# Performance work log

Measured on AMD Instinct MI355X. Metric: run time of the kernel, lower is better.

## Reference

```python
import jax, jax.numpy as jnp
import numpy as np

B, C, H, W = 16, 256, 128, 512
MINW, MINH, AF, HS = 128, 32, 256, 256


def _conv1d(x, w, b, pad):
    # x (B, Cin, L), w (Cout, Cin, K) -> (B, Cout, L)
    y = jax.lax.conv_general_dilated(x, w, (1,), [(pad, pad)],
                                     dimension_numbers=('NCH', 'OIH', 'NCH'))
    return y + b[None, :, None]


def setup_inputs() -> dict:
    key = jax.random.key(0)
    ks = jax.random.split(key, 22)
    def p(i, shape, s=0.05):
        return jax.random.normal(ks[i], shape, jnp.float32) * s
    return dict(
        features=jax.random.normal(ks[0], (B, C, H, W), jnp.float32),
        prev_attn_weights=jax.random.uniform(ks[1], (B, H), jnp.float32),
        coverage_vector=jax.random.uniform(ks[2], (B, H), jnp.float32) * 2.0,
        hidden=jax.random.normal(ks[3], (2, 1, B, HS), jnp.float32),
        dw_w=p(4, (MINW, 1)), dw_b=p(5, (1,)),
        enc_w=p(6, (C, AF)), enc_b=p(7, (AF,)),
        conv_w=p(8, (16, 2, 15)), conv_b=p(9, (16,)),
        dcb_w=p(10, (16, AF)), dcb_b=p(11, (AF,)),
        hid_w=p(12, (HS, AF)), hid_b=p(13, (AF,)),
        align_w=p(14, (AF, 1)), align_b=p(15, (1,)),
        convd_w=p(16, (AF, AF, 5)), convd_b=p(17, (AF,)),
        dh_w=p(18, (MINH, 1)), dh_b=p(19, (1,)),
        dec_w=p(20, (HS + AF, 2)), dec_b=p(21, (2,)),
    )


def reference(features, prev_attn_weights, coverage_vector, hidden,
              dw_w, dw_b, enc_w, enc_b, conv_w, conv_b, dcb_w, dcb_b,
              hid_w, hid_b, align_w, align_b, convd_w, convd_b,
              dh_w, dh_b, dec_w, dec_b):
    b, c, h, w = features.shape
    # AdaptiveMaxPool2d((None, MINW)): W divisible by MINW -> uniform windows
    pooled = features.reshape(b, c, h, MINW, w // MINW).max(-1)   # (B,C,H,MINW)
    h_feat = (pooled @ dw_w + dw_b)[..., 0]                       # (B,C,H)
    s = jnp.einsum('bch,cf->bhf', h_feat, enc_w) + enc_b          # (B,H,AF)
    # location + clamped coverage, InstanceNorm1d (no affine, eps=1e-5)
    cat = jnp.stack([prev_attn_weights,
                     jnp.clip(coverage_vector, 0.0, 1.0)], axis=1)  # (B,2,H)
    mu = cat.mean(-1, keepdims=True)
    var = cat.var(-1, keepdims=True)
    cat = (cat - mu) * jax.lax.rsqrt(var + 1e-5)
    cb = _conv1d(cat, conv_w, conv_b, 7)                          # (B,16,H)
    s = s + jnp.einsum('bkh,kf->bhf', cb, dcb_w) + dcb_b
    hh = hidden[0]                                                # (1,B,HS) = LSTM h
    s = s + (jnp.einsum('lbh,hf->lbf', hh, hid_w) + hid_b).transpose(1, 0, 2)  # (B,1,AF) bcast
    s = jnp.tanh(s)
    align = s @ align_w + align_b                                 # (B,H,1)
    attn = jax.nn.softmax(align, axis=1)[..., 0]                  # (B,H)
    context = jnp.einsum('bchw,bh->bcw', features, attn)          # (B,C,W)
    # learned stop decision
    d = jax.nn.relu(_conv1d(s.transpose(0, 2, 1), convd_w, convd_b, 2))  # (B,AF,H)
    d = d.reshape(b, AF, MINH, h // MINH).max(-1)                 # AdaptiveMaxPool1d(MINH)
    d = jax.nn.relu(d @ dh_w + dh_b)[..., 0]                      # (B,AF)
    d = jnp.concatenate([hh[0], d], axis=1)                       # (B,HS+AF)
    decision = d @ dec_w + dec_b                                  # (B,2)
    return context, attn, decision
```

## Files before the change

### kernel.cpp

```cpp
#include <hip/hip_runtime.h>
#include <hip/hip_bf16.h>
#include <math.h>

#define B_ 16
#define C_ 256
#define H_ 128
#define W_ 512
#define AF_ 256
#define HS_ 256

__global__ void k_pool(const float* __restrict__ feat,
                       const float* __restrict__ dw_w,
                       const float* __restrict__ dw_b,
                       float* __restrict__ hf) {
  int gid = blockIdx.x * blockDim.x + threadIdx.x;
  int wid = gid >> 6;
  int lane = threadIdx.x & 63;
  const float4* row = reinterpret_cast<const float4*>(feat) + (size_t)wid * 128;
  float4 a = row[lane];
  float4 b = row[lane + 64];
  float m0 = fmaxf(fmaxf(a.x, a.y), fmaxf(a.z, a.w));
  float m1 = fmaxf(fmaxf(b.x, b.y), fmaxf(b.z, b.w));
  float p = m0 * dw_w[lane] + m1 * dw_w[lane + 64];
#pragma unroll
  for (int off = 32; off > 0; off >>= 1) p += __shfl_down(p, off, 64);
  if (lane == 0) hf[wid] = p + dw_b[0];
}

__global__ void k_hid(const float* __restrict__ hidden,
                      const float* __restrict__ hid_w,
                      const float* __restrict__ hid_b,
                      float* __restrict__ hv) {
  int b = blockIdx.x, f = threadIdx.x;
  const float* hh = hidden + b * HS_;
  float acc = hid_b[f];
  for (int k = 0; k < HS_; ++k) acc = fmaf(hh[k], hid_w[k * AF_ + f], acc);
  hv[b * AF_ + f] = acc;
}

__global__ void k_sbuild(const float* __restrict__ pa,
                         const float* __restrict__ cv,
                         const float* __restrict__ hf,
                         const float* __restrict__ enc_w, const float* __restrict__ enc_b,
                         const float* __restrict__ conv_w, const float* __restrict__ conv_b,
                         const float* __restrict__ dcb_w, const float* __restrict__ dcb_b,
                         const float* __restrict__ hv,
                         const float* __restrict__ align_w, const float* __restrict__ align_b,
                         float* __restrict__ sbuf, float* __restrict__ alignv) {
  __shared__ float cat[2][H_];
  __shared__ float stats[4];
  __shared__ float cbl[4][16];
  __shared__ float red[4][4];
  int bidx = blockIdx.x;
  int b = bidx >> 5;
  int h0 = (bidx & 31) * 4;
  int tid = threadIdx.x;

  if (tid < H_) {
    cat[0][tid] = pa[b * H_ + tid];
    float x = cv[b * H_ + tid];
    cat[1][tid] = fminf(fmaxf(x, 0.f), 1.f);
  }
  __syncthreads();
  if (tid < 2) {
    float s = 0.f, s2 = 0.f;
    for (int t = 0; t < H_; ++t) { float x = cat[tid][t]; s += x; s2 += x * x; }
    float mu = s / (float)H_;
    float var = s2 / (float)H_ - mu * mu;
    stats[tid * 2] = mu;
    stats[tid * 2 + 1] = rsqrtf(var + 1e-5f);
  }
  __syncthreads();
  {
    int ch = tid >> 7, t = tid & 127;
    cat[ch][t] = (cat[ch][t] - stats[ch * 2]) * stats[ch * 2 + 1];
  }
  __syncthreads();
  if (tid < 64) {
    int k = tid & 15, j = tid >> 4;
    int h = h0 + j;
    float acc = conv_b[k];
    for (int c2 = 0; c2 < 2; ++c2)
      for (int t = 0; t < 15; ++t) {
        int hh = h + t - 7;
        if (hh >= 0 && hh < H_) acc += cat[c2][hh] * conv_w[(k * 2 + c2) * 15 + t];
      }
    cbl[j][k] = acc;
  }
  __syncthreads();

  int f = tid;
  float base = enc_b[f] + dcb_b[f] + hv[b * AF_ + f];
  float acc[4];
#pragma unroll
  for (int j = 0; j < 4; ++j) {
    float a = base;
#pragma unroll
    for (int k = 0; k < 16; ++k) a = fmaf(cbl[j][k], dcb_w[k * AF_ + f], a);
    acc[j] = a;
  }
  const float* hfb = hf + (size_t)(b * C_) * H_ + h0;
  for (int c = 0; c < C_; ++c) {
    float w = enc_w[c * AF_ + f];
#pragma unroll
    for (int j = 0; j < 4; ++j) acc[j] = fmaf(hfb[c * H_ + j], w, acc[j]);
  }
  float aw = align_w[f];
  int wv = tid >> 6, lane = tid & 63;
#pragma unroll
  for (int j = 0; j < 4; ++j) {
    float s = tanhf(acc[j]);
    sbuf[(size_t)(b * H_ + h0 + j) * AF_ + f] = s;
    float v = s * aw;
#pragma unroll
    for (int off = 32; off > 0; off >>= 1) v += __shfl_down(v, off, 64);
    if (lane == 0) red[wv][j] = v;
  }
  __syncthreads();
  if (tid < 4)
    alignv[b * H_ + h0 + tid] =
        red[0][tid] + red[1][tid] + red[2][tid] + red[3][tid] + align_b[0];
}

__global__ void k_softmax(const float* __restrict__ alignv, float* __restrict__ attn) {
  __shared__ float redm[2], reds[2];
  int b = blockIdx.x, t = threadIdx.x;
  float v = alignv[b * H_ + t];
  float m = v;
#pragma unroll
  for (int off = 32; off > 0; off >>= 1) m = fmaxf(m, __shfl_down(m, off, 64));
  if ((t & 63) == 0) redm[t >> 6] = m;
  __syncthreads();
  float mm = fmaxf(redm[0], redm[1]);
  float e = expf(v - mm);
  float s = e;
#pragma unroll
  for (int off = 32; off > 0; off >>= 1) s += __shfl_down(s, off, 64);
  if ((t & 63) == 0) reds[t >> 6] = s;
  __syncthreads();
  attn[b * H_ + t] = e / (reds[0] + reds[1]);
}

__global__ void k_wt(const float* __restrict__ convd_w, float* __restrict__ w2) {
  int f = blockIdx.x;
  int tid = threadIdx.x;
#pragma unroll
  for (int q = 0; q < 5; ++q) {
    int r = q * 256 + tid;
    w2[(size_t)r * 256 + f] = convd_w[(size_t)f * 1280 + r];
  }
}

__global__ void k_dconv(const float* __restrict__ sbuf, const float* __restrict__ w2,
                        const float* __restrict__ convd_b, float* __restrict__ dpool) {
  __shared__ float sw[12][AF_];
  __shared__ float part[8][AF_];
  int bidx = blockIdx.x;
  int b = bidx >> 4;
  int h0 = (bidx & 15) * 8;
  int tid = threadIdx.x;
  int f = tid & 255;
  int chalf = tid >> 8;
  for (int rr = chalf; rr < 12; rr += 2) {
    int h = h0 - 2 + rr;
    sw[rr][f] = (h >= 0 && h < H_) ? sbuf[(size_t)(b * H_ + h) * AF_ + f] : 0.f;
  }
  __syncthreads();
  float acc[8];
#pragma unroll
  for (int j = 0; j < 8; ++j) acc[j] = 0.f;
  int cstart = chalf * 128;
  for (int c = cstart; c < cstart + 128; ++c) {
    float sr[12];
#pragma unroll
    for (int rr = 0; rr < 12; ++rr) sr[rr] = sw[rr][c];
    const float* wp = w2 + (size_t)c * 5 * 256 + f;
#pragma unroll
    for (int t = 0; t < 5; ++t) {
      float wv = wp[t * 256];
#pragma unroll
      for (int j = 0; j < 8; ++j) acc[j] = fmaf(sr[j + t], wv, acc[j]);
    }
  }
  if (chalf == 1) {
#pragma unroll
    for (int j = 0; j < 8; ++j) part[j][f] = acc[j];
  }
  __syncthreads();
  if (chalf == 0) {
    float bias = convd_b[f];
#pragma unroll
    for (int j = 0; j < 8; ++j) acc[j] = fmaxf(acc[j] + part[j][f] + bias, 0.f);
    float p0 = fmaxf(fmaxf(acc[0], acc[1]), fmaxf(acc[2], acc[3]));
    float p1 = fmaxf(fmaxf(acc[4], acc[5]), fmaxf(acc[6], acc[7]));
    int m0 = h0 >> 2;
    dpool[(size_t)(b * 32 + m0) * AF_ + f] = p0;
    dpool[(size_t)(b * 32 + m0 + 1) * AF_ + f] = p1;
  }
}

__global__ void k_decision(const float* __restrict__ dpool, const float* __restrict__ hidden,
                           const float* __restrict__ dh_w, const float* __restrict__ dh_b,
                           const float* __restrict__ dec_w, const float* __restrict__ dec_b,
                           float* __restrict__ dec_out) {
  __shared__ float ddl[AF_];
  __shared__ float red[4];
  int b = blockIdx.x, tid = threadIdx.x;
  float acc = dh_b[0];
  for (int m = 0; m < 32; ++m) acc = fmaf(dpool[(size_t)(b * 32 + m) * AF_ + tid], dh_w[m], acc);
  ddl[tid] = fmaxf(acc, 0.f);
  __syncthreads();
  int col = tid >> 7, kk = tid & 127;
  float a = 0.f;
#pragma unroll
  for (int q = 0; q < 4; ++q) {
    int idx = kk + 128 * q;
    float x = (idx < 256) ? hidden[b * HS_ + idx] : ddl[idx - 256];
    a = fmaf(x, dec_w[idx * 2 + col], a);
  }
#pragma unroll
  for (int off = 32; off > 0; off >>= 1) a += __shfl_down(a, off, 64);
  if ((tid & 63) == 0) red[tid >> 6] = a;
  __syncthreads();
  if (tid < 2) dec_out[b * 2 + tid] = red[tid * 2] + red[tid * 2 + 1] + dec_b[tid];
}

__global__ void k_context(const float* __restrict__ feat, const float* __restrict__ attn,
                          float* __restrict__ ctx) {
  __shared__ float at[H_];
  int bidx = blockIdx.x;
  int b = bidx >> 7;
  int c0 = (bidx & 127) * 2;
  int tid = threadIdx.x;
  if (tid < H_) at[tid] = attn[b * H_ + tid];
  __syncthreads();
  int c = c0 + (tid >> 7);
  int wq = tid & 127;
  const float4* f4 = reinterpret_cast<const float4*>(feat) +
                     (size_t)(b * C_ + c) * H_ * (W_ / 4) + wq;
  float4 acc = make_float4(0.f, 0.f, 0.f, 0.f);
  for (int h = 0; h < H_; ++h) {
    float4 x = f4[(size_t)h * (W_ / 4)];
    float a = at[h];
    acc.x += x.x * a; acc.y += x.y * a; acc.z += x.z * a; acc.w += x.w * a;
  }
  reinterpret_cast<float4*>(ctx)[(size_t)(b * C_ + c) * (W_ / 4) + wq] = acc;
}

extern "C" void kernel_launch(void* const* d_in, const int* in_sizes, int n_in,
                              void* d_out, int out_size, void* d_ws, size_t ws_size,
                              hipStream_t stream) {
  const float* feat    = (const float*)d_in[0];
  const float* pa      = (const float*)d_in[1];
  const float* cv      = (const float*)d_in[2];
  const float* hidden  = (const float*)d_in[3];
  const float* dw_w    = (const float*)d_in[4];
  const float* dw_b    = (const float*)d_in[5];
  const float* enc_w   = (const float*)d_in[6];
  const float* enc_b   = (const float*)d_in[7];
  const float* conv_w  = (const float*)d_in[8];
  const float* conv_b  = (const float*)d_in[9];
  const float* dcb_w   = (const float*)d_in[10];
  const float* dcb_b   = (const float*)d_in[11];
  const float* hid_w   = (const float*)d_in[12];
  const float* hid_b   = (const float*)d_in[13];
  const float* align_w = (const float*)d_in[14];
  const float* align_b = (const float*)d_in[15];
  const float* convd_w = (const float*)d_in[16];
  const float* convd_b = (const float*)d_in[17];
  const float* dh_w    = (const float*)d_in[18];
  const float* dh_b    = (const float*)d_in[19];
  const float* dec_w   = (const float*)d_in[20];
  const float* dec_b   = (const float*)d_in[21];

  float* out  = (float*)d_out;
  float* ctx  = out;
  float* attn = out + 2097152;
  float* dec  = out + 2097152 + 2048;

  float* hf     = ctx;
  float* sbuf   = ctx + 524288;
  float* dpool  = ctx + 1048576;
  float* hv     = ctx + 1179648;
  float* alignv = ctx + 1183744;
  float* w2     = ctx + 1185792;

  k_pool<<<131072, 256, 0, stream>>>(feat, dw_w, dw_b, hf);
  k_hid<<<16, 256, 0, stream>>>(hidden, hid_w, hid_b, hv);
  k_sbuild<<<512, 256, 0, stream>>>(pa, cv, hf, enc_w, enc_b, conv_w, conv_b,
                                    dcb_w, dcb_b, hv, align_w, align_b, sbuf, alignv);
  k_softmax<<<16, 128, 0, stream>>>(alignv, attn);
  k_wt<<<256, 256, 0, stream>>>(convd_w, w2);
  k_dconv<<<256, 512, 0, stream>>>(sbuf, w2, convd_b, dpool);
  k_decision<<<16, 256, 0, stream>>>(dpool, hidden, dh_w, dh_b, dec_w, dec_b, dec);
  k_context<<<2048, 256, 0, stream>>>(feat, attn, ctx);
}
```

Measured before the change: 442.7 us.

## Fuse small kernels, batch pool rows per wave, stage pooled features in LDS

```diff
diff --git a/kernel.cpp b/kernel.cpp
--- a/kernel.cpp
+++ b/kernel.cpp
@@ -9,33 +9,50 @@
 #define AF_ 256
 #define HS_ 256
 
+__global__ void k_pre(const float* __restrict__ convd_w,
+                      const float* __restrict__ hidden,
+                      const float* __restrict__ hid_w,
+                      const float* __restrict__ hid_b,
+                      float* __restrict__ w2, float* __restrict__ hv) {
+  int bid = blockIdx.x, tid = threadIdx.x;
+  if (bid < 256) {
+    int f = bid;
+#pragma unroll
+    for (int q = 0; q < 5; ++q) {
+      int r = q * 256 + tid;
+      w2[(size_t)r * 256 + f] = convd_w[(size_t)f * 1280 + r];
+    }
+  } else {
+    int b = bid - 256;
+    const float* hh = hidden + b * HS_;
+    float acc = hid_b[tid];
+    for (int k = 0; k < HS_; ++k) acc = fmaf(hh[k], hid_w[k * AF_ + tid], acc);
+    hv[b * AF_ + tid] = acc;
+  }
+}
+
 __global__ void k_pool(const float* __restrict__ feat,
                        const float* __restrict__ dw_w,
                        const float* __restrict__ dw_b,
                        float* __restrict__ hf) {
   int gid = blockIdx.x * blockDim.x + threadIdx.x;
-  int wid = gid >> 6;
+  int wv = gid >> 6;
   int lane = threadIdx.x & 63;
-  const float4* row = reinterpret_cast<const float4*>(feat) + (size_t)wid * 128;
-  float4 a = row[lane];
-  float4 b = row[lane + 64];
-  float m0 = fmaxf(fmaxf(a.x, a.y), fmaxf(a.z, a.w));
-  float m1 = fmaxf(fmaxf(b.x, b.y), fmaxf(b.z, b.w));
-  float p = m0 * dw_w[lane] + m1 * dw_w[lane + 64];
-#pragma unroll
-  for (int off = 32; off > 0; off >>= 1) p += __shfl_down(p, off, 64);
-  if (lane == 0) hf[wid] = p + dw_b[0];
-}
-
-__global__ void k_hid(const float* __restrict__ hidden,
-                      const float* __restrict__ hid_w,
-                      const float* __restrict__ hid_b,
-                      float* __restrict__ hv) {
-  int b = blockIdx.x, f = threadIdx.x;
-  const float* hh = hidden + b * HS_;
-  float acc = hid_b[f];
-  for (int k = 0; k < HS_; ++k) acc = fmaf(hh[k], hid_w[k * AF_ + f], acc);
-  hv[b * AF_ + f] = acc;
+  int base_row = wv * 32;
+  float w0 = dw_w[lane], w1 = dw_w[lane + 64], wb = dw_b[0];
+  const float4* f4 = reinterpret_cast<const float4*>(feat);
+#pragma unroll 4
+  for (int r = 0; r < 32; ++r) {
+    const float4* row = f4 + (size_t)(base_row + r) * 128;
+    float4 a = row[lane];
+    float4 b = row[lane + 64];
+    float m0 = fmaxf(fmaxf(a.x, a.y), fmaxf(a.z, a.w));
+    float m1 = fmaxf(fmaxf(b.x, b.y), fmaxf(b.z, b.w));
+    float p = m0 * w0 + m1 * w1;
+#pragma unroll
+    for (int off = 32; off > 0; off >>= 1) p += __shfl_down(p, off, 64);
+    if (lane == 0) hf[base_row + r] = p + wb;
+  }
 }
 
 __global__ void k_sbuild(const float* __restrict__ pa,
@@ -51,11 +68,21 @@
   __shared__ float stats[4];
   __shared__ float cbl[4][16];
   __shared__ float red[4][4];
+  __shared__ float4 hfl[C_];
   int bidx = blockIdx.x;
   int b = bidx >> 5;
   int h0 = (bidx & 31) * 4;
   int tid = threadIdx.x;
 
+  {
+    float* hl = reinterpret_cast<float*>(hfl);
+#pragma unroll
+    for (int q = 0; q < 4; ++q) {
+      int t = tid + q * 256;
+      int c = t >> 2, j = t & 3;
+      hl[t] = hf[(size_t)(b * C_ + c) * H_ + h0 + j];
+    }
+  }
   if (tid < H_) {
     cat[0][tid] = pa[b * H_ + tid];
     float x = cv[b * H_ + tid];
@@ -99,14 +126,16 @@
     for (int k = 0; k < 16; ++k) a = fmaf(cbl[j][k], dcb_w[k * AF_ + f], a);
     acc[j] = a;
   }
-  const float* hfb = hf + (size_t)(b * C_) * H_ + h0;
   for (int c = 0; c < C_; ++c) {
     float w = enc_w[c * AF_ + f];
-#pragma unroll
-    for (int j = 0; j < 4; ++j) acc[j] = fmaf(hfb[c * H_ + j], w, acc[j]);
+    float4 h4 = hfl[c];
+    acc[0] = fmaf(h4.x, w, acc[0]);
+    acc[1] = fmaf(h4.y, w, acc[1]);
+    acc[2] = fmaf(h4.z, w, acc[2]);
+    acc[3] = fmaf(h4.w, w, acc[3]);
   }
   float aw = align_w[f];
-  int wv = tid >> 6, lane = tid & 63;
+  int wvi = tid >> 6, lane = tid & 63;
 #pragma unroll
   for (int j = 0; j < 4; ++j) {
     float s = tanhf(acc[j]);
@@ -114,7 +143,7 @@
     float v = s * aw;
 #pragma unroll
     for (int off = 32; off > 0; off >>= 1) v += __shfl_down(v, off, 64);
-    if (lane == 0) red[wv][j] = v;
+    if (lane == 0) red[wvi][j] = v;
   }
   __syncthreads();
   if (tid < 4)
@@ -141,61 +170,64 @@
   attn[b * H_ + t] = e / (reds[0] + reds[1]);
 }
 
-__global__ void k_wt(const float* __restrict__ convd_w, float* __restrict__ w2) {
-  int f = blockIdx.x;
+__global__ void k_ctx_dconv(const float* __restrict__ feat, const float* __restrict__ attn,
+                            const float* __restrict__ sbuf, const float* __restrict__ w2,
+                            const float* __restrict__ convd_b,
+                            float* __restrict__ dpool, float* __restrict__ ctx) {
+  __shared__ float sw[12][AF_];
+  int bidx = blockIdx.x;
   int tid = threadIdx.x;
-#pragma unroll
-  for (int q = 0; q < 5; ++q) {
-    int r = q * 256 + tid;
-    w2[(size_t)r * 256 + f] = convd_w[(size_t)f * 1280 + r];
-  }
-}
-
-__global__ void k_dconv(const float* __restrict__ sbuf, const float* __restrict__ w2,
-                        const float* __restrict__ convd_b, float* __restrict__ dpool) {
-  __shared__ float sw[12][AF_];
-  __shared__ float part[8][AF_];
-  int bidx = blockIdx.x;
-  int b = bidx >> 4;
-  int h0 = (bidx & 15) * 8;
-  int tid = threadIdx.x;
-  int f = tid & 255;
-  int chalf = tid >> 8;
-  for (int rr = chalf; rr < 12; rr += 2) {
-    int h = h0 - 2 + rr;
-    sw[rr][f] = (h >= 0 && h < H_) ? sbuf[(size_t)(b * H_ + h) * AF_ + f] : 0.f;
-  }
-  __syncthreads();
-  float acc[8];
-#pragma unroll
-  for (int j = 0; j < 8; ++j) acc[j] = 0.f;
-  int cstart = chalf * 128;
-  for (int c = cstart; c < cstart + 128; ++c) {
-    float sr[12];
-#pragma unroll
-    for (int rr = 0; rr < 12; ++rr) sr[rr] = sw[rr][c];
-    const float* wp = w2 + (size_t)c * 5 * 256 + f;
-#pragma unroll
-    for (int t = 0; t < 5; ++t) {
-      float wv = wp[t * 256];
-#pragma unroll
-      for (int j = 0; j < 8; ++j) acc[j] = fmaf(sr[j + t], wv, acc[j]);
-    }
-  }
-  if (chalf == 1) {
-#pragma unroll
-    for (int j = 0; j < 8; ++j) part[j][f] = acc[j];
-  }
-  __syncthreads();
-  if (chalf == 0) {
+  if (bidx < 256) {
+    int b = bidx >> 4;
+    int h0 = (bidx & 15) * 8;
+    int f = tid;
+    for (int rr = 0; rr < 12; ++rr) {
+      int h = h0 - 2 + rr;
+      sw[rr][f] = (h >= 0 && h < H_) ? sbuf[(size_t)(b * H_ + h) * AF_ + f] : 0.f;
+    }
+    __syncthreads();
+    float acc[8];
+#pragma unroll
+    for (int j = 0; j < 8; ++j) acc[j] = 0.f;
+    for (int c = 0; c < C_; ++c) {
+      float sr[12];
+#pragma unroll
+      for (int rr = 0; rr < 12; ++rr) sr[rr] = sw[rr][c];
+      const float* wp = w2 + (size_t)c * 5 * 256 + f;
+#pragma unroll
+      for (int t = 0; t < 5; ++t) {
+        float wvv = wp[t * 256];
+#pragma unroll
+        for (int j = 0; j < 8; ++j) acc[j] = fmaf(sr[j + t], wvv, acc[j]);
+      }
+    }
     float bias = convd_b[f];
 #pragma unroll
-    for (int j = 0; j < 8; ++j) acc[j] = fmaxf(acc[j] + part[j][f] + bias, 0.f);
+    for (int j = 0; j < 8; ++j) acc[j] = fmaxf(acc[j] + bias, 0.f);
     float p0 = fmaxf(fmaxf(acc[0], acc[1]), fmaxf(acc[2], acc[3]));
     float p1 = fmaxf(fmaxf(acc[4], acc[5]), fmaxf(acc[6], acc[7]));
-    int m0 = h0 >> 2;
+    int m0 = (h0 >> 2);
     dpool[(size_t)(b * 32 + m0) * AF_ + f] = p0;
     dpool[(size_t)(b * 32 + m0 + 1) * AF_ + f] = p1;
+  } else {
+    int cb = bidx - 256;
+    int b = cb >> 7;
+    int c0 = (cb & 127) * 2;
+    float* at = &sw[0][0];
+    if (tid < H_) at[tid] = attn[b * H_ + tid];
+    __syncthreads();
+    int c = c0 + (tid >> 7);
+    int wq = tid & 127;
+    const float4* f4 = reinterpret_cast<const float4*>(feat) +
+                       (size_t)(b * C_ + c) * H_ * (W_ / 4) + wq;
+    float4 acc = make_float4(0.f, 0.f, 0.f, 0.f);
+#pragma unroll 4
+    for (int h = 0; h < H_; ++h) {
+      float4 x = f4[(size_t)h * (W_ / 4)];
+      float a = at[h];
+      acc.x += x.x * a; acc.y += x.y * a; acc.z += x.z * a; acc.w += x.w * a;
+    }
+    reinterpret_cast<float4*>(ctx)[(size_t)(b * C_ + c) * (W_ / 4) + wq] = acc;
   }
 }
 
@@ -223,28 +255,6 @@
   if ((tid & 63) == 0) red[tid >> 6] = a;
   __syncthreads();
   if (tid < 2) dec_out[b * 2 + tid] = red[tid * 2] + red[tid * 2 + 1] + dec_b[tid];
-}
-
-__global__ void k_context(const float* __restrict__ feat, const float* __restrict__ attn,
-                          float* __restrict__ ctx) {
-  __shared__ float at[H_];
-  int bidx = blockIdx.x;
-  int b = bidx >> 7;
-  int c0 = (bidx & 127) * 2;
-  int tid = threadIdx.x;
-  if (tid < H_) at[tid] = attn[b * H_ + tid];
-  __syncthreads();
-  int c = c0 + (tid >> 7);
-  int wq = tid & 127;
-  const float4* f4 = reinterpret_cast<const float4*>(feat) +
-                     (size_t)(b * C_ + c) * H_ * (W_ / 4) + wq;
-  float4 acc = make_float4(0.f, 0.f, 0.f, 0.f);
-  for (int h = 0; h < H_; ++h) {
-    float4 x = f4[(size_t)h * (W_ / 4)];
-    float a = at[h];
-    acc.x += x.x * a; acc.y += x.y * a; acc.z += x.z * a; acc.w += x.w * a;
-  }
-  reinterpret_cast<float4*>(ctx)[(size_t)(b * C_ + c) * (W_ / 4) + wq] = acc;
 }
 
 extern "C" void kernel_launch(void* const* d_in, const int* in_sizes, int n_in,
@@ -278,20 +288,19 @@
   float* attn = out + 2097152;
   float* dec  = out + 2097152 + 2048;
 
-  float* hf     = ctx;
-  float* sbuf   = ctx + 524288;
-  float* dpool  = ctx + 1048576;
-  float* hv     = ctx + 1179648;
-  float* alignv = ctx + 1183744;
-  float* w2     = ctx + 1185792;
-
-  k_pool<<<131072, 256, 0, stream>>>(feat, dw_w, dw_b, hf);
-  k_hid<<<16, 256, 0, stream>>>(hidden, hid_w, hid_b, hv);
+  float* ws     = (float*)d_ws;
+  float* hf     = ws;
+  float* sbuf   = ws + 524288;
+  float* dpool  = ws + 1048576;
+  float* hv     = ws + 1179648;
+  float* alignv = ws + 1183744;
+  float* w2     = ws + 1185792;
+
+  k_pre<<<272, 256, 0, stream>>>(convd_w, hidden, hid_w, hid_b, w2, hv);
+  k_pool<<<4096, 256, 0, stream>>>(feat, dw_w, dw_b, hf);
   k_sbuild<<<512, 256, 0, stream>>>(pa, cv, hf, enc_w, enc_b, conv_w, conv_b,
                                     dcb_w, dcb_b, hv, align_w, align_b, sbuf, alignv);
   k_softmax<<<16, 128, 0, stream>>>(alignv, attn);
-  k_wt<<<256, 256, 0, stream>>>(convd_w, w2);
-  k_dconv<<<256, 512, 0, stream>>>(sbuf, w2, convd_b, dpool);
+  k_ctx_dconv<<<2304, 256, 0, stream>>>(feat, attn, sbuf, w2, convd_b, dpool, ctx);
   k_decision<<<16, 256, 0, stream>>>(dpool, hidden, dh_w, dh_b, dec_w, dec_b, dec);
-  k_context<<<2048, 256, 0, stream>>>(feat, attn, ctx);
-}
+}
```

Result: slower. 490.2 us (+10.7%).
